# Kernel optimization log

Hardware: AMD Instinct MI355X
Metric: run time of the kernel (lower is better)

Reference implementation:

```python
import jax, jax.numpy as jnp
import numpy as np

ROWS, COLS = 4, 4
B, N = 8192, 64


def setup_inputs() -> dict:
    key = jax.random.key(0)
    k1, k2 = jax.random.split(key)
    # Scale uniform entries down so colsum(x^5)^4 stays well inside fp32 range.
    x = jax.random.uniform(k1, (B, N, N), dtype=jnp.float32) * 0.2
    # kaiming_normal_ on a (rows, cols) param: std = sqrt(2 / fan_in), fan_in = cols
    coef = jax.random.normal(k2, (ROWS, COLS), dtype=jnp.float32) * np.sqrt(2.0 / COLS)
    return {"x": x, "coef": coef}


def _forward(x, coef):
    rows, cols = coef.shape
    x = x.astype(jnp.float32)
    if x.ndim == 2:
        x = x[None]
    # Incremental matrix powers: p_i = x^(i+2), i = 0..rows-1 (the only powers
    # consumed by nout; the extra power computed in nas is dead code).
    p0 = jnp.matmul(x, x)  # x^2, [B, n, n]
    def step(p, _):
        p = jnp.matmul(x, p)
        return p, p
    if rows > 1:
        _, rest = jax.lax.scan(step, p0, None, length=rows - 1)
        powers = jnp.concatenate([p0[None], rest], axis=0)  # [rows, B, n, n]
    else:
        powers = p0[None]
    # ones[n,n] @ P has every row equal to the column sums of P, so
    # trace((ones @ P) ** (j+1)) = sum_k colsum_k(P) ** (j+1).
    colsums = powers.sum(axis=-2)  # [rows, B, n]
    exps = jnp.arange(1, cols + 1, dtype=jnp.float32)  # j + 1
    traces = jnp.sum(colsums[:, None, :, :] ** exps[None, :, None, None], axis=-1)  # [rows, cols, B]
    traces = jnp.transpose(traces, (2, 0, 1))  # [B, rows, cols]
    # nnorm: numel = rows*cols (numel of a single [rows,cols] trace matrix),
    # raised to (i + j + 2)
    pow_mat = (jnp.arange(rows, dtype=jnp.float32)[:, None]
               + jnp.arange(cols, dtype=jnp.float32)[None, :] + 2.0)
    norm = jnp.asarray(rows * cols, jnp.float32) ** pow_mat  # [rows, cols]
    return (coef * traces / norm).sum(axis=(-1, -2))  # [B]


def reference(x, coef):
    return _forward(x, coef)
```

## Files before the change

kernel.cpp:

```cpp
#include <hip/hip_runtime.h>


#define WPB 4

typedef float vf4 __attribute__((ext_vector_type(4)));

__device__ __forceinline__ vf4 xor_reduce_rg(vf4 v) {
    v.x += __shfl_xor(v.x, 16, 64); v.y += __shfl_xor(v.y, 16, 64);
    v.z += __shfl_xor(v.z, 16, 64); v.w += __shfl_xor(v.w, 16, 64);
    v.x += __shfl_xor(v.x, 32, 64); v.y += __shfl_xor(v.y, 32, 64);
    v.z += __shfl_xor(v.z, 32, 64); v.w += __shfl_xor(v.w, 32, 64);
    return v;
}

__global__ __launch_bounds__(256) void nufa_kernel(
    const float* __restrict__ x, const float* __restrict__ coef,
    float* __restrict__ out, int B)
{
    const int wave = threadIdx.x >> 6;
    const int lane = threadIdx.x & 63;
    const int b    = blockIdx.x * WPB + wave;
    if (b >= B) return;

    const int rg = lane >> 4;
    const int cg = lane & 15;

    __shared__ float us[WPB][4][64];

    const vf4* xb = reinterpret_cast<const vf4*>(x) + (size_t)b * 1024;

    vf4 xr[16];
    #pragma unroll
    for (int i = 0; i < 16; ++i)
        xr[i] = __builtin_nontemporal_load(xb + 64 * i + lane);

    float cs[4][4];
    #pragma unroll
    for (int i = 0; i < 4; ++i)
        #pragma unroll
        for (int j = 0; j < 4; ++j)
            cs[i][j] = coef[i * 4 + j] * (1.0f / (float)(1ull << (4 * (i + j + 2))));

    vf4 u = xr[0];
    #pragma unroll
    for (int i = 1; i < 16; ++i) u += xr[i];
    u = xor_reduce_rg(u);

    if (rg == 0) *reinterpret_cast<vf4*>(&us[wave][0][4 * cg]) = u;

    float contrib = 0.f;
    #pragma unroll
    for (int m = 0; m < 4; ++m) {
        __syncthreads();
        const float* uslot = &us[wave][m][rg];
        vf4 acc = {0.f, 0.f, 0.f, 0.f};
        #pragma unroll
        for (int i = 0; i < 16; ++i) {
            const float uk = uslot[4 * i];
            acc += uk * xr[i];
        }
        u = xor_reduce_rg(acc);
        if (m < 3 && rg == 0)
            *reinterpret_cast<vf4*>(&us[wave][m + 1][4 * cg]) = u;

        #pragma unroll
        for (int c = 0; c < 4; ++c) {
            const float v1 = (c == 0) ? u.x : (c == 1) ? u.y : (c == 2) ? u.z : u.w;
            const float v2 = v1 * v1;
            const float v3 = v2 * v1;
            const float v4 = v2 * v2;
            contrib += cs[m][0] * v1 + cs[m][1] * v2 + cs[m][2] * v3 + cs[m][3] * v4;
        }
    }

    #pragma unroll
    for (int d = 1; d < 16; d <<= 1) contrib += __shfl_xor(contrib, d, 64);
    if (lane == 0) out[b] = contrib;
}

extern "C" void kernel_launch(void* const* d_in, const int* in_sizes, int n_in,
                              void* d_out, int out_size, void* d_ws, size_t ws_size,
                              hipStream_t stream) {
    const float* x    = (const float*)d_in[0];
    const float* coef = (const float*)d_in[1];
    float* out        = (float*)d_out;
    const int B = in_sizes[0] / 4096;
    const int blocks = (B + WPB - 1) / WPB;
    nufa_kernel<<<blocks, 256, 0, stream>>>(x, coef, out, B);
}
```

Measured before the change: 27.37 us.

## Stream batches into LDS with async global_load_lds and process several per wave

Each wave now handles four consecutive batch matrices instead of one. It uses direct global-to-LDS loads to stage the next 16 KB matrix while it computes the current one, so memory traffic overlaps with the power-series reduction. Blocks shrink to two waves with a per-wave LDS slot, and the block-wide __syncthreads is dropped because the reduction scratch is now wave-private. This cuts the number of waves in flight and raises LDS use per block, which could reduce memory-level parallelism in a kernel that is bandwidth-bound.

```diff
diff --git a/kernel.cpp b/kernel.cpp
--- a/kernel.cpp
+++ b/kernel.cpp
@@ -1,7 +1,7 @@
 #include <hip/hip_runtime.h>
 
 
-#define WPB 4
+#define NB 4
 
 typedef float vf4 __attribute__((ext_vector_type(4)));
 
@@ -13,26 +13,32 @@
     return v;
 }
 
-__global__ __launch_bounds__(256) void nufa_kernel(
+__device__ __forceinline__ void stage_batch(const float* g, float* ls, int lane) {
+    #pragma unroll
+    for (int i = 0; i < 16; ++i) {
+        __builtin_amdgcn_global_load_lds(
+            (const __attribute__((address_space(1))) void*)(g + i * 256 + lane * 4),
+            (__attribute__((address_space(3))) void*)(ls + i * 256),
+            16, 0, 0);
+    }
+}
+
+__global__ __launch_bounds__(128) void nufa_kernel(
     const float* __restrict__ x, const float* __restrict__ coef,
     float* __restrict__ out, int B)
 {
-    const int wave = threadIdx.x >> 6;
+    __shared__ float slot[2][4096];
+    __shared__ float us[2][4][64];
+
+    const int w    = threadIdx.x >> 6;
     const int lane = threadIdx.x & 63;
-    const int b    = blockIdx.x * WPB + wave;
-    if (b >= B) return;
+    const int rg   = lane >> 4;
+    const int cg   = lane & 15;
+    const int b0   = (blockIdx.x * 2 + w) * NB;
+    if (b0 >= B) return;
 
-    const int rg = lane >> 4;
-    const int cg = lane & 15;
-
-    __shared__ float us[WPB][4][64];
-
-    const vf4* xb = reinterpret_cast<const vf4*>(x) + (size_t)b * 1024;
-
-    vf4 xr[16];
-    #pragma unroll
-    for (int i = 0; i < 16; ++i)
-        xr[i] = __builtin_nontemporal_load(xb + 64 * i + lane);
+    float* ls = &slot[w][0];
+    const float* xb = x + (size_t)b0 * 4096;
 
     float cs[4][4];
     #pragma unroll
@@ -41,41 +47,56 @@
         for (int j = 0; j < 4; ++j)
             cs[i][j] = coef[i * 4 + j] * (1.0f / (float)(1ull << (4 * (i + j + 2))));
 
-    vf4 u = xr[0];
+    stage_batch(xb, ls, lane);
+
     #pragma unroll
-    for (int i = 1; i < 16; ++i) u += xr[i];
-    u = xor_reduce_rg(u);
+    for (int it = 0; it < NB; ++it) {
+        asm volatile("s_waitcnt vmcnt(0)" ::: "memory");
+        __builtin_amdgcn_sched_barrier(0);
 
-    if (rg == 0) *reinterpret_cast<vf4*>(&us[wave][0][4 * cg]) = u;
+        vf4 xr[16];
+        #pragma unroll
+        for (int k = 0; k < 16; ++k)
+            xr[k] = *reinterpret_cast<const vf4*>(ls + k * 256 + lane * 4);
 
-    float contrib = 0.f;
-    #pragma unroll
-    for (int m = 0; m < 4; ++m) {
-        __syncthreads();
-        const float* uslot = &us[wave][m][rg];
-        vf4 acc = {0.f, 0.f, 0.f, 0.f};
+        asm volatile("s_waitcnt lgkmcnt(0)" ::: "memory");
+        __builtin_amdgcn_sched_barrier(0);
+        if (it + 1 < NB) stage_batch(xb + (size_t)(it + 1) * 4096, ls, lane);
+
+        vf4 u = xr[0];
         #pragma unroll
-        for (int i = 0; i < 16; ++i) {
-            const float uk = uslot[4 * i];
-            acc += uk * xr[i];
+        for (int k = 1; k < 16; ++k) u += xr[k];
+        u = xor_reduce_rg(u);
+
+        if (rg == 0) *reinterpret_cast<vf4*>(&us[w][0][4 * cg]) = u;
+
+        float contrib = 0.f;
+        #pragma unroll
+        for (int m = 0; m < 4; ++m) {
+            const float* uslot = &us[w][m][rg];
+            vf4 acc = {0.f, 0.f, 0.f, 0.f};
+            #pragma unroll
+            for (int i = 0; i < 16; ++i) acc += uslot[4 * i] * xr[i];
+            u = xor_reduce_rg(acc);
+            if (m < 3 && rg == 0)
+                *reinterpret_cast<vf4*>(&us[w][m + 1][4 * cg]) = u;
+
+            #pragma unroll
+            for (int c = 0; c < 4; ++c) {
+                const float v1 = (c == 0) ? u.x : (c == 1) ? u.y
+                               : (c == 2) ? u.z : u.w;
+                const float v2 = v1 * v1;
+                const float v3 = v2 * v1;
+                const float v4 = v2 * v2;
+                contrib += cs[m][0] * v1 + cs[m][1] * v2
+                         + cs[m][2] * v3 + cs[m][3] * v4;
+            }
         }
-        u = xor_reduce_rg(acc);
-        if (m < 3 && rg == 0)
-            *reinterpret_cast<vf4*>(&us[wave][m + 1][4 * cg]) = u;
 
         #pragma unroll
-        for (int c = 0; c < 4; ++c) {
-            const float v1 = (c == 0) ? u.x : (c == 1) ? u.y : (c == 2) ? u.z : u.w;
-            const float v2 = v1 * v1;
-            const float v3 = v2 * v1;
-            const float v4 = v2 * v2;
-            contrib += cs[m][0] * v1 + cs[m][1] * v2 + cs[m][2] * v3 + cs[m][3] * v4;
-        }
+        for (int d = 1; d < 16; d <<= 1) contrib += __shfl_xor(contrib, d, 64);
+        if (lane == 0) out[b0 + it] = contrib;
     }
-
-    #pragma unroll
-    for (int d = 1; d < 16; d <<= 1) contrib += __shfl_xor(contrib, d, 64);
-    if (lane == 0) out[b] = contrib;
 }
 
 extern "C" void kernel_launch(void* const* d_in, const int* in_sizes, int n_in,
@@ -85,6 +106,7 @@
     const float* coef = (const float*)d_in[1];
     float* out        = (float*)d_out;
     const int B = in_sizes[0] / 4096;
-    const int blocks = (B + WPB - 1) / WPB;
-    nufa_kernel<<<blocks, 256, 0, stream>>>(x, coef, out, B);
+    const int waves  = (B + NB - 1) / NB;
+    const int blocks = (waves + 1) / 2;
+    nufa_kernel<<<blocks, 128, 0, stream>>>(x, coef, out, B);
 }
```

Measured after the change: 29.24 us. 1.07x slower.

## Assign one column per lane and broadcast vector via readlane

Applied to the files above, without the earlier changes.

Each lane now keeps one full column of the 64x64 matrix (64 scalar loads, stride 64) in place of float4 row fragments. The column-sum vector is shared across lanes with scalar readlane broadcasts, which drops the LDS staging, the __syncthreads calls and the cross-row shuffle reductions. The trade-off is scalar loads that are no longer float4 or nontemporal, and 64 serial readlanes per power step, which may add scalar-unit latency.

```diff
diff --git a/kernel.cpp b/kernel.cpp
--- a/kernel.cpp
+++ b/kernel.cpp
@@ -1,16 +1,8 @@
 #include <hip/hip_runtime.h>
 
 
-#define WPB 4
-
-typedef float vf4 __attribute__((ext_vector_type(4)));
-
-__device__ __forceinline__ vf4 xor_reduce_rg(vf4 v) {
-    v.x += __shfl_xor(v.x, 16, 64); v.y += __shfl_xor(v.y, 16, 64);
-    v.z += __shfl_xor(v.z, 16, 64); v.w += __shfl_xor(v.w, 16, 64);
-    v.x += __shfl_xor(v.x, 32, 64); v.y += __shfl_xor(v.y, 32, 64);
-    v.z += __shfl_xor(v.z, 32, 64); v.w += __shfl_xor(v.w, 32, 64);
-    return v;
+__device__ __forceinline__ float rdlane(float v, int i) {
+    return __int_as_float(__builtin_amdgcn_readlane(__float_as_int(v), i));
 }
 
 __global__ __launch_bounds__(256) void nufa_kernel(
@@ -19,62 +11,49 @@
 {
     const int wave = threadIdx.x >> 6;
     const int lane = threadIdx.x & 63;
-    const int b    = blockIdx.x * WPB + wave;
+    const int b    = blockIdx.x * 4 + wave;
     if (b >= B) return;
 
-    const int rg = lane >> 4;
-    const int cg = lane & 15;
-
-    __shared__ float us[WPB][4][64];
-
-    const vf4* xb = reinterpret_cast<const vf4*>(x) + (size_t)b * 1024;
-
-    vf4 xr[16];
+    const float* xb = x + (size_t)b * 4096 + lane;
+    float xr[64];
     #pragma unroll
-    for (int i = 0; i < 16; ++i)
-        xr[i] = __builtin_nontemporal_load(xb + 64 * i + lane);
+    for (int i = 0; i < 64; ++i) xr[i] = xb[i * 64];
 
     float cs[4][4];
     #pragma unroll
-    for (int i = 0; i < 4; ++i)
+    for (int m = 0; m < 4; ++m)
         #pragma unroll
         for (int j = 0; j < 4; ++j)
-            cs[i][j] = coef[i * 4 + j] * (1.0f / (float)(1ull << (4 * (i + j + 2))));
+            cs[m][j] = coef[m * 4 + j] * (1.0f / (float)(1ull << (4 * (m + j + 2))));
 
-    vf4 u = xr[0];
+    float s0 = xr[0], s1 = xr[1], s2 = xr[2], s3 = xr[3],
+          s4 = xr[4], s5 = xr[5], s6 = xr[6], s7 = xr[7];
     #pragma unroll
-    for (int i = 1; i < 16; ++i) u += xr[i];
-    u = xor_reduce_rg(u);
-
-    if (rg == 0) *reinterpret_cast<vf4*>(&us[wave][0][4 * cg]) = u;
+    for (int i = 8; i < 64; i += 8) {
+        s0 += xr[i];     s1 += xr[i + 1]; s2 += xr[i + 2]; s3 += xr[i + 3];
+        s4 += xr[i + 4]; s5 += xr[i + 5]; s6 += xr[i + 6]; s7 += xr[i + 7];
+    }
+    float u = ((s0 + s1) + (s2 + s3)) + ((s4 + s5) + (s6 + s7));
 
     float contrib = 0.f;
     #pragma unroll
     for (int m = 0; m < 4; ++m) {
-        __syncthreads();
-        const float* uslot = &us[wave][m][rg];
-        vf4 acc = {0.f, 0.f, 0.f, 0.f};
+        float a0 = 0.f, a1 = 0.f, a2 = 0.f, a3 = 0.f;
         #pragma unroll
-        for (int i = 0; i < 16; ++i) {
-            const float uk = uslot[4 * i];
-            acc += uk * xr[i];
+        for (int i = 0; i < 64; i += 4) {
+            a0 = __builtin_fmaf(rdlane(u, i + 0), xr[i + 0], a0);
+            a1 = __builtin_fmaf(rdlane(u, i + 1), xr[i + 1], a1);
+            a2 = __builtin_fmaf(rdlane(u, i + 2), xr[i + 2], a2);
+            a3 = __builtin_fmaf(rdlane(u, i + 3), xr[i + 3], a3);
         }
-        u = xor_reduce_rg(acc);
-        if (m < 3 && rg == 0)
-            *reinterpret_cast<vf4*>(&us[wave][m + 1][4 * cg]) = u;
+        u = (a0 + a1) + (a2 + a3);
 
-        #pragma unroll
-        for (int c = 0; c < 4; ++c) {
-            const float v1 = (c == 0) ? u.x : (c == 1) ? u.y : (c == 2) ? u.z : u.w;
-            const float v2 = v1 * v1;
-            const float v3 = v2 * v1;
-            const float v4 = v2 * v2;
-            contrib += cs[m][0] * v1 + cs[m][1] * v2 + cs[m][2] * v3 + cs[m][3] * v4;
-        }
+        const float v1 = u, v2 = u * u, v3 = v2 * u, v4 = v2 * v2;
+        contrib += cs[m][0] * v1 + cs[m][1] * v2 + cs[m][2] * v3 + cs[m][3] * v4;
     }
 
     #pragma unroll
-    for (int d = 1; d < 16; d <<= 1) contrib += __shfl_xor(contrib, d, 64);
+    for (int d = 1; d < 64; d <<= 1) contrib += __shfl_xor(contrib, d, 64);
     if (lane == 0) out[b] = contrib;
 }
 
@@ -85,6 +64,6 @@
     const float* coef = (const float*)d_in[1];
     float* out        = (float*)d_out;
     const int B = in_sizes[0] / 4096;
-    const int blocks = (B + WPB - 1) / WPB;
+    const int blocks = (B + 3) / 4;
     nufa_kernel<<<blocks, 256, 0, stream>>>(x, coef, out, B);
 }
```

Result: faster. 26.29 us (-3.9%).
